# Optimization experiments

Measured on AMD Instinct MI355X. Metric: run time of the kernel, lower is better.

The kernel has to match this reference:

```python
import jax, jax.numpy as jnp
import numpy as np

B, C, H, W = 4, 128, 100, 256
M = 2

def setup_inputs() -> dict:
    key = jax.random.key(0)
    ks = jax.random.split(key, 5)
    feat0 = jax.random.normal(ks[0], (B, C, H, W), jnp.float32)
    feat1 = jax.random.normal(ks[1], (B, C, H, W), jnp.float32)
    adapter_weight = jax.random.normal(ks[2], (M, C), jnp.float32)
    # conv: 1x1 Conv2d(M*C -> C); store as [C_out, C_in]
    conv_w = jax.random.normal(ks[3], (C, M * C), jnp.float32) * (1.0 / np.sqrt(M * C))
    conv_b = jnp.zeros((C,), jnp.float32)
    mlp_w = jax.random.normal(ks[4], (C, C), jnp.float32) * (1.0 / np.sqrt(C))
    mlp_b = jnp.zeros((C,), jnp.float32)
    return {"feat0": feat0, "feat1": feat1, "adapter_weight": adapter_weight,
            "conv_w": conv_w, "conv_b": conv_b, "mlp_w": mlp_w, "mlp_b": mlp_b}

def reference(feat0, feat1, adapter_weight, conv_w, conv_b, mlp_w, mlp_b):
    feats = jnp.stack([feat0, feat1], axis=0)              # [M, B, C, H, W]
    b, c, h, w = feat0.shape
    # per-modality scalar-per-channel scale, then concat on channel dim
    scaled = feats * adapter_weight[:, None, :, None, None]
    cat = scaled.transpose(1, 0, 2, 3, 4).reshape(b, -1, h, w)  # [B, M*C, H, W]
    # 1x1 conv == channel matmul
    fused = jnp.einsum('bkhw,ck->bchw', cat, conv_w) + conv_b[None, :, None, None]
    f = fused.transpose(2, 3, 0, 1).reshape(h * w, b, c)   # [(HW), B, C]
    fm = feats.transpose(0, 3, 4, 1, 2).reshape(len(feats), h * w, b, c)  # [M, (HW), B, C]
    # per-location cross-agent attention, summed over modalities
    scores = jnp.einsum('msbc,sdc->msbd', fm, f) / np.sqrt(c).astype(jnp.float32)
    attn = jax.nn.softmax(scores, axis=-1)                 # [M, (HW), B, B]
    retrieved = jnp.einsum('msbd,sdc->sbc', attn, f)       # summed over m
    out = f + jax.nn.relu(retrieved @ mlp_w.T + mlp_b)
    return out.reshape(h, w, b, c).transpose(2, 3, 0, 1)   # [B, C, H, W]
```

## Files before the change

kernel.cpp:

```cpp
#include <hip/hip_runtime.h>

#define HW 25600
#define TS 16
#define NT 1600
#define NB 256

typedef float  f32x4   __attribute__((ext_vector_type(4)));
typedef short  short8  __attribute__((ext_vector_type(8)));
typedef short  short4v __attribute__((ext_vector_type(4)));
typedef unsigned int uint2v __attribute__((ext_vector_type(2)));
typedef unsigned int uint4v __attribute__((ext_vector_type(4)));

__device__ __forceinline__ float bf2f(short h) {
    return __builtin_bit_cast(float, (unsigned)((unsigned short)h) << 16);
}
__device__ __forceinline__ unsigned cvt_pk(float a, float b) {
    unsigned r;
    asm("v_cvt_pk_bf16_f32 %0, %1, %2" : "=v"(r) : "v"(a), "v"(b));
    return r;
}

typedef __attribute__((address_space(3))) const char lds_cchar;
typedef __attribute__((address_space(3))) char lds_char;
typedef __attribute__((address_space(1))) const void g_cvoid;
__device__ __forceinline__ unsigned lds_u32(const void* p) {
    return (unsigned)(uintptr_t)(lds_cchar*)p;
}
__device__ __forceinline__ void dma16(const float* g, unsigned lds_byte) {
    __builtin_amdgcn_global_load_lds(
        (g_cvoid*)g,
        (__attribute__((address_space(3))) void*)(lds_char*)(uintptr_t)lds_byte,
        16, 0, 0);
}

__device__ __forceinline__ short4v tr_read(unsigned a) {
    short4v d;
    asm volatile("ds_read_b64_tr_b16 %0, %1" : "=v"(d) : "v"(a) : "memory");
    return d;
}
__device__ __forceinline__ short4v tr_read128(unsigned a) {
    short4v d;
    asm volatile("ds_read_b64_tr_b16 %0, %1 offset:128" : "=v"(d) : "v"(a) : "memory");
    return d;
}
__device__ __forceinline__ uint4v lds_b128(unsigned a) {
    uint4v d;
    asm volatile("ds_read_b128 %0, %1" : "=v"(d) : "v"(a) : "memory");
    return d;
}
__device__ __forceinline__ void wait_lgkm8() {
    asm volatile("s_waitcnt lgkmcnt(8)" ::: "memory");
    __builtin_amdgcn_sched_barrier(0);
}
__device__ __forceinline__ void wait_lgkm6() {
    asm volatile("s_waitcnt lgkmcnt(6)" ::: "memory");
    __builtin_amdgcn_sched_barrier(0);
}
__device__ __forceinline__ void wait_lgkm4() {
    asm volatile("s_waitcnt lgkmcnt(4)" ::: "memory");
    __builtin_amdgcn_sched_barrier(0);
}
__device__ __forceinline__ void wait_lgkm0() {
    asm volatile("s_waitcnt lgkmcnt(0)" ::: "memory");
    __builtin_amdgcn_sched_barrier(0);
}
__device__ __forceinline__ void wait_vm0() {
    asm volatile("s_waitcnt vmcnt(0)" ::: "memory");
    __builtin_amdgcn_sched_barrier(0);
}
__device__ __forceinline__ void bar_lgkm() {
    asm volatile("s_waitcnt lgkmcnt(0)" ::: "memory");
    __builtin_amdgcn_s_barrier();
    asm volatile("" ::: "memory");
}

struct Clu { short4v lo0, hi0, lo1, hi1, lo2, hi2, lo3, hi3; };
__device__ __forceinline__ void issue_clu(Clu& C, unsigned base, int tstride) {
    C.lo0 = tr_read(base);                C.hi0 = tr_read128(base);
    C.lo1 = tr_read(base + tstride);      C.hi1 = tr_read128(base + tstride);
    C.lo2 = tr_read(base + 2 * tstride);  C.hi2 = tr_read128(base + 2 * tstride);
    C.lo3 = tr_read(base + 3 * tstride);  C.hi3 = tr_read128(base + 3 * tstride);
}
__device__ __forceinline__ short8 mk8(short4v lo, short4v hi) {
    return __builtin_shufflevector(lo, hi, 0, 1, 2, 3, 4, 5, 6, 7);
}

__global__ __launch_bounds__(512, 2) void mmf_kernel(
    const float* __restrict__ feat0, const float* __restrict__ feat1,
    const float* __restrict__ adapter, const float* __restrict__ conv_w,
    const float* __restrict__ conv_b, const float* __restrict__ mlp_w,
    const float* __restrict__ mlp_b, float* __restrict__ out)
{
    __shared__ __align__(128) char smem[116736];
    float* Xf32 = (float*)smem;
    short* Xbf  = (short*)(smem + 65536);
    short* fbf  = (short*)(smem + 98304);
    float* sc   = (float*)(smem + 114688);

    const int tid = threadIdx.x;
    const int bid = blockIdx.x;
    const int xcd  = bid & 7;
    const int jb   = bid >> 3;
    const int tbeg = 200 * xcd + jb;
    const int tend = 200 * (xcd + 1);
    const int w   = __builtin_amdgcn_readfirstlane(tid >> 6);
    const int l   = tid & 63;
    const int g   = l >> 4;
    const int sl  = l & 15;
    const int c0  = w * 16;

    const unsigned xfbase = lds_u32(Xf32);
    const unsigned xbase  = lds_u32(Xbf);
    const unsigned fbase  = lds_u32(fbf);

    auto stage_dma = [&](int S) {
        #pragma unroll
        for (int i = 0; i < 8; ++i) {
            int idx = i * 512 + tid;
            int q  = idx & 3;
            int r  = idx >> 2;
            int cc = r & 127;
            int b  = (r >> 7) & 3;
            int m  = r >> 9;
            const float* fp = m ? feat1 : feat0;
            dma16(fp + (size_t)((b * 128 + cc) * HW + S + q * 4),
                  xfbase + (unsigned)((i * 512 + (w << 6)) << 4));
        }
    };

    stage_dma(tbeg * TS);

    short8 afc[8];
    #pragma unroll
    for (int ks = 0; ks < 8; ++ks) {
        const int k0 = ks * 32 + g * 8;
        const float4 w0 = *reinterpret_cast<const float4*>(conv_w + (c0 + sl) * 256 + k0);
        const float4 w1 = *reinterpret_cast<const float4*>(conv_w + (c0 + sl) * 256 + k0 + 4);
        const float4 a0 = *reinterpret_cast<const float4*>(adapter + k0);
        const float4 a1 = *reinterpret_cast<const float4*>(adapter + k0 + 4);
        uint4v au;
        au[0] = cvt_pk(w0.x * a0.x, w0.y * a0.y);
        au[1] = cvt_pk(w0.z * a0.z, w0.w * a0.w);
        au[2] = cvt_pk(w1.x * a1.x, w1.y * a1.y);
        au[3] = cvt_pk(w1.z * a1.z, w1.w * a1.w);
        afc[ks] = __builtin_bit_cast(short8, au);
    }
    short8 afm[4];
    #pragma unroll
    for (int ks = 0; ks < 4; ++ks) {
        const int k0 = ks * 32 + g * 8;
        const float4 w0 = *reinterpret_cast<const float4*>(mlp_w + (c0 + sl) * 128 + k0);
        const float4 w1 = *reinterpret_cast<const float4*>(mlp_w + (c0 + sl) * 128 + k0 + 4);
        uint4v au;
        au[0] = cvt_pk(w0.x, w0.y);
        au[1] = cvt_pk(w0.z, w0.w);
        au[2] = cvt_pk(w1.x, w1.y);
        au[3] = cvt_pk(w1.z, w1.w);
        afm[ks] = __builtin_bit_cast(short8, au);
    }
    float bias[4], mb[4];
    #pragma unroll
    for (int i = 0; i < 4; ++i) {
        bias[i] = conv_b[c0 + g * 4 + i];
        mb[i]   = mlp_b[c0 + g * 4 + i];
    }
    wait_vm0();
    bar_lgkm();

    for (int ti = tbeg; ti < tend; ti += 32) {
        const int S = ti * TS;

        #pragma unroll
        for (int i = 0; i < 8; ++i) {
            int idx = i * 512 + tid;
            const float4 v = *reinterpret_cast<const float4*>(Xf32 + (size_t)idx * 4);
            int q  = idx & 3;
            int r  = idx >> 2;
            int cc = r & 127;
            int b  = (r >> 7) & 3;
            int m  = r >> 9;
            uint2v xv;
            xv[0] = cvt_pk(v.x, v.y);
            xv[1] = cvt_pk(v.z, v.w);
            *reinterpret_cast<uint2v*>(Xbf + b * 4096 + (m * 128 + cc) * 16 + q * 4) = xv;
        }
        bar_lgkm();

        if (ti + 32 < tend) stage_dma((ti + 32) * TS);

        {
            f32x4 acc[4] = {{0,0,0,0},{0,0,0,0},{0,0,0,0},{0,0,0,0}};
            Clu cA, cB;
            issue_clu(cA, xbase + 0 * 1024 + g * 256 + sl * 8, 8192);
            #pragma unroll
            for (int ks = 0; ks < 8; ++ks) {
                Clu& cur = (ks & 1) ? cB : cA;
                Clu& nxt = (ks & 1) ? cA : cB;
                if (ks < 7) {
                    issue_clu(nxt, xbase + (ks + 1) * 1024 + g * 256 + sl * 8, 8192);
                    wait_lgkm8();
                } else {
                    wait_lgkm0();
                }
                acc[0] = __builtin_amdgcn_mfma_f32_16x16x32_bf16(afc[ks], mk8(cur.lo0, cur.hi0), acc[0], 0, 0, 0);
                acc[1] = __builtin_amdgcn_mfma_f32_16x16x32_bf16(afc[ks], mk8(cur.lo1, cur.hi1), acc[1], 0, 0, 0);
                acc[2] = __builtin_amdgcn_mfma_f32_16x16x32_bf16(afc[ks], mk8(cur.lo2, cur.hi2), acc[2], 0, 0, 0);
                acc[3] = __builtin_amdgcn_mfma_f32_16x16x32_bf16(afc[ks], mk8(cur.lo3, cur.hi3), acc[3], 0, 0, 0);
            }
            #pragma unroll
            for (int tt = 0; tt < 4; ++tt) {
                const int col = tt * 16 + sl;
                uint2v fu;
                fu[0] = cvt_pk(acc[tt][0] + bias[0], acc[tt][1] + bias[1]);
                fu[1] = cvt_pk(acc[tt][2] + bias[2], acc[tt][3] + bias[3]);
                *reinterpret_cast<uint2v*>(fbf + col * 128 + (((c0 + g * 4) ^ (sl << 3)) ^ (tt << 5))) = fu;
            }
        }
        bar_lgkm();

        f32x4 gacc[4] = {{0,0,0,0},{0,0,0,0},{0,0,0,0},{0,0,0,0}};
        {
            const int sm_m = w >> 2;
            const int sm_b = w & 3;
            const int ad = sl >> 2;
            const int aq = sl & 3;
            const unsigned btile = xbase + sm_b * 8192 + sm_m * 4096 + g * 256 + sl * 8;
            f32x4 accS[4] = {{0,0,0,0},{0,0,0,0},{0,0,0,0},{0,0,0,0}};
            struct SC { short4v blo, bhi; uint4v a0, a1, a2, a3; };
            SC pA, pB;
            auto issue = [&](SC& Sv, int kk) {
                const unsigned bt = btile + (unsigned)(kk * 1024);
                Sv.blo = tr_read(bt); Sv.bhi = tr_read128(bt);
                const int cg = kk * 4 + g;
                Sv.a0 = lds_b128(fbase + (unsigned)((ad * 16 + 0 + aq) * 256 + (((cg ^ (0 + aq)) ^ (ad << 2)) << 4)));
                Sv.a1 = lds_b128(fbase + (unsigned)((ad * 16 + 4 + aq) * 256 + (((cg ^ (4 + aq)) ^ (ad << 2)) << 4)));
                Sv.a2 = lds_b128(fbase + (unsigned)((ad * 16 + 8 + aq) * 256 + (((cg ^ (8 + aq)) ^ (ad << 2)) << 4)));
                Sv.a3 = lds_b128(fbase + (unsigned)((ad * 16 + 12 + aq) * 256 + (((cg ^ (12 + aq)) ^ (ad << 2)) << 4)));
            };
            issue(pA, 0);
            #pragma unroll
            for (int kk = 0; kk < 4; ++kk) {
                SC& cur = (kk & 1) ? pB : pA;
                SC& nxt = (kk & 1) ? pA : pB;
                if (kk < 3) {
                    issue(nxt, kk + 1);
                    wait_lgkm6();
                } else {
                    wait_lgkm0();
                }
                const short8 bf = mk8(cur.blo, cur.bhi);
                accS[0] = __builtin_amdgcn_mfma_f32_16x16x32_bf16(__builtin_bit_cast(short8, cur.a0), bf, accS[0], 0, 0, 0);
                accS[1] = __builtin_amdgcn_mfma_f32_16x16x32_bf16(__builtin_bit_cast(short8, cur.a1), bf, accS[1], 0, 0, 0);
                accS[2] = __builtin_amdgcn_mfma_f32_16x16x32_bf16(__builtin_bit_cast(short8, cur.a2), bf, accS[2], 0, 0, 0);
                accS[3] = __builtin_amdgcn_mfma_f32_16x16x32_bf16(__builtin_bit_cast(short8, cur.a3), bf, accS[3], 0, 0, 0);
            }
            const int cstar = sl >> 2, qstar = sl & 3;
            float x = accS[0][0];
            #pragma unroll
            for (int c = 0; c < 4; ++c)
                #pragma unroll
                for (int q = 0; q < 4; ++q)
                    if (c == cstar && q == qstar) x = accS[c][q];
            x *= 0.088388347648318447f;
            float mx = fmaxf(x, __shfl_xor(x, 16));
            mx = fmaxf(mx, __shfl_xor(mx, 32));
            float e = __expf(x - mx);
            float sm = e + __shfl_xor(e, 16);
            sm += __shfl_xor(sm, 32);
            sc[(sm_m * 16 + sm_b * 4 + g) * 16 + sl] = e / sm;

            struct Qu { uint4v q0, q1, q2, q3; };
            Qu qA, qB;
            auto issue_q = [&](Qu& Q, int ks) {
                const int cb = ks * 4 + g;
                Q.q0 = lds_b128(fbase + (unsigned)((0 * 16 + sl) * 256 + (((cb ^ sl) ^ 0)  << 4)));
                Q.q1 = lds_b128(fbase + (unsigned)((1 * 16 + sl) * 256 + (((cb ^ sl) ^ 4)  << 4)));
                Q.q2 = lds_b128(fbase + (unsigned)((2 * 16 + sl) * 256 + (((cb ^ sl) ^ 8)  << 4)));
                Q.q3 = lds_b128(fbase + (unsigned)((3 * 16 + sl) * 256 + (((cb ^ sl) ^ 12) << 4)));
            };
            issue_q(qA, 0);
            #pragma unroll
            for (int ks = 0; ks < 4; ++ks) {
                Qu& cur = (ks & 1) ? qB : qA;
                Qu& nxt = (ks & 1) ? qA : qB;
                if (ks < 3) {
                    issue_q(nxt, ks + 1);
                    wait_lgkm4();
                } else {
                    wait_lgkm0();
                }
                gacc[0] = __builtin_amdgcn_mfma_f32_16x16x32_bf16(afm[ks], __builtin_bit_cast(short8, cur.q0), gacc[0], 0, 0, 0);
                gacc[1] = __builtin_amdgcn_mfma_f32_16x16x32_bf16(afm[ks], __builtin_bit_cast(short8, cur.q1), gacc[1], 0, 0, 0);
                gacc[2] = __builtin_amdgcn_mfma_f32_16x16x32_bf16(afm[ks], __builtin_bit_cast(short8, cur.q2), gacc[2], 0, 0, 0);
                gacc[3] = __builtin_amdgcn_mfma_f32_16x16x32_bf16(afm[ks], __builtin_bit_cast(short8, cur.q3), gacc[3], 0, 0, 0);
            }
        }
        bar_lgkm();

        {
            float aw_[4][4];
            #pragma unroll
            for (int b = 0; b < 4; ++b)
                #pragma unroll
                for (int d = 0; d < 4; ++d)
                    aw_[b][d] = sc[(b * 4 + d) * 16 + sl] + sc[256 + (b * 4 + d) * 16 + sl];
            wait_vm0();
            #pragma unroll
            for (int b = 0; b < 4; ++b) {
                const int col = b * 16 + sl;
                const short4v res = *reinterpret_cast<const short4v*>(
                    fbf + col * 128 + (((c0 + g * 4) ^ (sl << 3)) ^ (b << 5)));
                #pragma unroll
                for (int i = 0; i < 4; ++i) {
                    float v = mb[i];
                    #pragma unroll
                    for (int d = 0; d < 4; ++d) v += aw_[b][d] * gacc[d][i];
                    const int c = c0 + g * 4 + i;
                    out[(size_t)(b * 128 + c) * HW + S + sl] =
                        fmaxf(v, 0.f) + bf2f(res[i]);
                }
            }
        }
    }
}

extern "C" void kernel_launch(void* const* d_in, const int* in_sizes, int n_in,
                              void* d_out, int out_size, void* d_ws, size_t ws_size,
                              hipStream_t stream) {
    const float* feat0   = (const float*)d_in[0];
    const float* feat1   = (const float*)d_in[1];
    const float* adapter = (const float*)d_in[2];
    const float* conv_w  = (const float*)d_in[3];
    const float* conv_b  = (const float*)d_in[4];
    const float* mlp_w   = (const float*)d_in[5];
    const float* mlp_b   = (const float*)d_in[6];
    float* out = (float*)d_out;

    dim3 grid(NB);
    dim3 block(512);
    hipLaunchKernelGGL(mmf_kernel, grid, block, 0, stream,
                       feat0, feat1, adapter, conv_w, conv_b, mlp_w, mlp_b, out);
}
```

Measured before the change: 44.47 us.

## Retile conv GEMM per wave to 32 channels x 2 batches, halving LDS reads

The 1x1-conv MFMA stage is retiled so each wave computes a 32-output-channel by 2-batch block instead of 16 channels by 4 batches. Each B fragment read from LDS is now reused across two A fragments, which halves the transposed LDS reads per wave. The cost is twice as many conv weight registers. The launch-bounds occupancy hint drops from 2 to 1 blocks per CU to make room for them.

```diff
diff --git a/kernel.cpp b/kernel.cpp
--- a/kernel.cpp
+++ b/kernel.cpp
@@ -48,10 +48,6 @@
     asm volatile("ds_read_b128 %0, %1" : "=v"(d) : "v"(a) : "memory");
     return d;
 }
-__device__ __forceinline__ void wait_lgkm8() {
-    asm volatile("s_waitcnt lgkmcnt(8)" ::: "memory");
-    __builtin_amdgcn_sched_barrier(0);
-}
 __device__ __forceinline__ void wait_lgkm6() {
     asm volatile("s_waitcnt lgkmcnt(6)" ::: "memory");
     __builtin_amdgcn_sched_barrier(0);
@@ -74,18 +70,16 @@
     asm volatile("" ::: "memory");
 }
 
-struct Clu { short4v lo0, hi0, lo1, hi1, lo2, hi2, lo3, hi3; };
-__device__ __forceinline__ void issue_clu(Clu& C, unsigned base, int tstride) {
+struct Clu2 { short4v lo0, hi0, lo1, hi1; };
+__device__ __forceinline__ void issue_clu2(Clu2& C, unsigned base, int tstride) {
     C.lo0 = tr_read(base);                C.hi0 = tr_read128(base);
     C.lo1 = tr_read(base + tstride);      C.hi1 = tr_read128(base + tstride);
-    C.lo2 = tr_read(base + 2 * tstride);  C.hi2 = tr_read128(base + 2 * tstride);
-    C.lo3 = tr_read(base + 3 * tstride);  C.hi3 = tr_read128(base + 3 * tstride);
 }
 __device__ __forceinline__ short8 mk8(short4v lo, short4v hi) {
     return __builtin_shufflevector(lo, hi, 0, 1, 2, 3, 4, 5, 6, 7);
 }
 
-__global__ __launch_bounds__(512, 2) void mmf_kernel(
+__global__ __launch_bounds__(512, 1) void mmf_kernel(
     const float* __restrict__ feat0, const float* __restrict__ feat1,
     const float* __restrict__ adapter, const float* __restrict__ conv_w,
     const float* __restrict__ conv_b, const float* __restrict__ mlp_w,
@@ -108,6 +102,8 @@
     const int g   = l >> 4;
     const int sl  = l & 15;
     const int c0  = w * 16;
+    const int wc  = w >> 1;
+    const int wb  = w & 1;
 
     const unsigned xfbase = lds_u32(Xf32);
     const unsigned xbase  = lds_u32(Xbf);
@@ -130,20 +126,24 @@
 
     stage_dma(tbeg * TS);
 
-    short8 afc[8];
+    short8 afc2[2][8];
     #pragma unroll
-    for (int ks = 0; ks < 8; ++ks) {
-        const int k0 = ks * 32 + g * 8;
-        const float4 w0 = *reinterpret_cast<const float4*>(conv_w + (c0 + sl) * 256 + k0);
-        const float4 w1 = *reinterpret_cast<const float4*>(conv_w + (c0 + sl) * 256 + k0 + 4);
-        const float4 a0 = *reinterpret_cast<const float4*>(adapter + k0);
-        const float4 a1 = *reinterpret_cast<const float4*>(adapter + k0 + 4);
-        uint4v au;
-        au[0] = cvt_pk(w0.x * a0.x, w0.y * a0.y);
-        au[1] = cvt_pk(w0.z * a0.z, w0.w * a0.w);
-        au[2] = cvt_pk(w1.x * a1.x, w1.y * a1.y);
-        au[3] = cvt_pk(w1.z * a1.z, w1.w * a1.w);
-        afc[ks] = __builtin_bit_cast(short8, au);
+    for (int cc2 = 0; cc2 < 2; ++cc2) {
+        const int crow = wc * 32 + cc2 * 16 + sl;
+        #pragma unroll
+        for (int ks = 0; ks < 8; ++ks) {
+            const int k0 = ks * 32 + g * 8;
+            const float4 w0 = *reinterpret_cast<const float4*>(conv_w + crow * 256 + k0);
+            const float4 w1 = *reinterpret_cast<const float4*>(conv_w + crow * 256 + k0 + 4);
+            const float4 a0 = *reinterpret_cast<const float4*>(adapter + k0);
+            const float4 a1 = *reinterpret_cast<const float4*>(adapter + k0 + 4);
+            uint4v au;
+            au[0] = cvt_pk(w0.x * a0.x, w0.y * a0.y);
+            au[1] = cvt_pk(w0.z * a0.z, w0.w * a0.w);
+            au[2] = cvt_pk(w1.x * a1.x, w1.y * a1.y);
+            au[3] = cvt_pk(w1.z * a1.z, w1.w * a1.w);
+            afc2[cc2][ks] = __builtin_bit_cast(short8, au);
+        }
     }
     short8 afm[4];
     #pragma unroll
@@ -158,12 +158,14 @@
         au[3] = cvt_pk(w1.z, w1.w);
         afm[ks] = __builtin_bit_cast(short8, au);
     }
-    float bias[4], mb[4];
+    float bias2[2][4], mb[4];
     #pragma unroll
-    for (int i = 0; i < 4; ++i) {
-        bias[i] = conv_b[c0 + g * 4 + i];
-        mb[i]   = mlp_b[c0 + g * 4 + i];
-    }
+    for (int cc2 = 0; cc2 < 2; ++cc2)
+        #pragma unroll
+        for (int i = 0; i < 4; ++i)
+            bias2[cc2][i] = conv_b[wc * 32 + cc2 * 16 + g * 4 + i];
+    #pragma unroll
+    for (int i = 0; i < 4; ++i) mb[i] = mlp_b[c0 + g * 4 + i];
     wait_vm0();
     bar_lgkm();
 
@@ -189,31 +191,41 @@
         if (ti + 32 < tend) stage_dma((ti + 32) * TS);
 
         {
-            f32x4 acc[4] = {{0,0,0,0},{0,0,0,0},{0,0,0,0},{0,0,0,0}};
-            Clu cA, cB;
-            issue_clu(cA, xbase + 0 * 1024 + g * 256 + sl * 8, 8192);
+            f32x4 a00 = {0,0,0,0}, a01 = {0,0,0,0};
+            f32x4 a10 = {0,0,0,0}, a11 = {0,0,0,0};
+            const unsigned cb0 = xbase + (unsigned)(wb * 16384) + g * 256 + sl * 8;
+            Clu2 cA, cB;
+            issue_clu2(cA, cb0, 8192);
             #pragma unroll
             for (int ks = 0; ks < 8; ++ks) {
-                Clu& cur = (ks & 1) ? cB : cA;
-                Clu& nxt = (ks & 1) ? cA : cB;
+                Clu2& cur = (ks & 1) ? cB : cA;
+                Clu2& nxt = (ks & 1) ? cA : cB;
                 if (ks < 7) {
-                    issue_clu(nxt, xbase + (ks + 1) * 1024 + g * 256 + sl * 8, 8192);
-                    wait_lgkm8();
+                    issue_clu2(nxt, cb0 + (unsigned)((ks + 1) * 1024), 8192);
+                    wait_lgkm4();
                 } else {
                     wait_lgkm0();
                 }
-                acc[0] = __builtin_amdgcn_mfma_f32_16x16x32_bf16(afc[ks], mk8(cur.lo0, cur.hi0), acc[0], 0, 0, 0);
-                acc[1] = __builtin_amdgcn_mfma_f32_16x16x32_bf16(afc[ks], mk8(cur.lo1, cur.hi1), acc[1], 0, 0, 0);
-                acc[2] = __builtin_amdgcn_mfma_f32_16x16x32_bf16(afc[ks], mk8(cur.lo2, cur.hi2), acc[2], 0, 0, 0);
-                acc[3] = __builtin_amdgcn_mfma_f32_16x16x32_bf16(afc[ks], mk8(cur.lo3, cur.hi3), acc[3], 0, 0, 0);
-            }
-            #pragma unroll
-            for (int tt = 0; tt < 4; ++tt) {
-                const int col = tt * 16 + sl;
-                uint2v fu;
-                fu[0] = cvt_pk(acc[tt][0] + bias[0], acc[tt][1] + bias[1]);
-                fu[1] = cvt_pk(acc[tt][2] + bias[2], acc[tt][3] + bias[3]);
-                *reinterpret_cast<uint2v*>(fbf + col * 128 + (((c0 + g * 4) ^ (sl << 3)) ^ (tt << 5))) = fu;
+                const short8 b0 = mk8(cur.lo0, cur.hi0);
+                const short8 b1 = mk8(cur.lo1, cur.hi1);
+                a00 = __builtin_amdgcn_mfma_f32_16x16x32_bf16(afc2[0][ks], b0, a00, 0, 0, 0);
+                a01 = __builtin_amdgcn_mfma_f32_16x16x32_bf16(afc2[0][ks], b1, a01, 0, 0, 0);
+                a10 = __builtin_amdgcn_mfma_f32_16x16x32_bf16(afc2[1][ks], b0, a10, 0, 0, 0);
+                a11 = __builtin_amdgcn_mfma_f32_16x16x32_bf16(afc2[1][ks], b1, a11, 0, 0, 0);
+            }
+            #pragma unroll
+            for (int cc2 = 0; cc2 < 2; ++cc2) {
+                const int cX = wc * 32 + cc2 * 16 + g * 4;
+                #pragma unroll
+                for (int bb = 0; bb < 2; ++bb) {
+                    const f32x4& ac = cc2 ? (bb ? a11 : a10) : (bb ? a01 : a00);
+                    const int b   = wb * 2 + bb;
+                    const int col = b * 16 + sl;
+                    uint2v fu;
+                    fu[0] = cvt_pk(ac[0] + bias2[cc2][0], ac[1] + bias2[cc2][1]);
+                    fu[1] = cvt_pk(ac[2] + bias2[cc2][2], ac[3] + bias2[cc2][3]);
+                    *reinterpret_cast<uint2v*>(fbf + col * 128 + ((cX ^ (sl << 3)) ^ (b << 5))) = fu;
+                }
             }
         }
         bar_lgkm();
```

Result: slower. 53.11 us (+19.4%).
